# Optimization experiments

Hardware: AMD Instinct MI355X
Metric: run time of the kernel (lower is better)

Reference implementation:

```python
import jax, jax.numpy as jnp
import numpy as np

NEG_INF = -1e30


def _rope_interleaved(x, freqs):
    # x: [B,S,H,D], freqs broadcastable [1,S,1,D]; interleaved even/odd rotation
    x0 = x[..., 0::2]
    x1 = x[..., 1::2]
    f0 = freqs[..., 0::2]
    f1 = freqs[..., 1::2]
    o0 = f0 * x0 - f1 * x1
    o1 = f1 * x0 + f0 * x1
    # interleave back: out[...,0::2]=o0, out[...,1::2]=o1
    out = jnp.stack([o0, o1], axis=-1)  # [B,S,H,D/2,2]
    return out.reshape(x.shape).astype(x.dtype)


def setup_inputs() -> dict:
    key = jax.random.key(0)
    kq, kk, kv, kf = jax.random.split(key, 4)
    B, S, H, D = 2, 2048, 16, 128
    q = jax.random.normal(kq, (B, S, H, D), dtype=jnp.float32)
    k = jax.random.normal(kk, (B, S, H, D), dtype=jnp.float32)
    v = jax.random.normal(kv, (B, S, H, D), dtype=jnp.float32)
    freqs = jax.random.normal(kf, (1, S, 1, D), dtype=jnp.float32)
    return {"q": q, "k": k, "v": v, "freqs": freqs}


def reference(q, k, v, freqs):
    # RoPE (Wan-style indexed interleaved write) on q and k
    rq = _rope_interleaved(q, freqs)  # [B,S,H,D]
    rk = _rope_interleaved(k, freqs)
    B, S, H, D = q.shape
    scale = 1.0 / jnp.sqrt(jnp.asarray(D, dtype=q.dtype))
    # transpose(1,2) -> [B,H,S,D]; fused into einsum subscripts
    scores = jnp.einsum("bqhd,bkhd->bhqk", rq, rk) * scale  # [B,H,S,S]
    causal = jnp.tril(jnp.ones((S, S), dtype=bool))
    scores = jnp.where(causal[None, None, :, :], scores, NEG_INF)
    probs = jax.nn.softmax(scores, axis=-1)
    out = jnp.einsum("bhqk,bkhd->bhqd", probs, v)  # [B,H,S,D]
    return out
```

## Files before the change

### kernel.cpp

```cpp
#include <hip/hip_runtime.h>
#include <hip/hip_bf16.h>

#define B_  2
#define S_  2048
#define H_  16
#define D_  128
#define BQ  128
#define SH  (H_ * D_)
#define NT  (S_ / 64)
#define NTQ (S_ / BQ)
#define TILE_US 8192

typedef __attribute__((ext_vector_type(8))) short bf16x8;
typedef __attribute__((ext_vector_type(4))) float f32x4;
typedef __attribute__((ext_vector_type(4))) unsigned int u32x4;

__device__ __forceinline__ ushort f2bf(float x) {
  union { float f; unsigned u; } c; c.f = x;
  unsigned u = c.u;
  return (ushort)((u + 0x7FFFu + ((u >> 16) & 1u)) >> 16);
}

__device__ __forceinline__ void gload_lds16(const ushort* g, ushort* l) {
  __builtin_amdgcn_global_load_lds((const __attribute__((address_space(1))) void*)g,
                                   (__attribute__((address_space(3))) void*)l,
                                   16, 0, 0);
}

__device__ __forceinline__ bf16x8 ntload8(const ushort* p) {
  union { u32x4 u; bf16x8 v; } c;
  c.u = __builtin_nontemporal_load((const u32x4*)p);
  return c.v;
}

__device__ __forceinline__ unsigned cvt_pk_bf16(float lo, float hi) {
  unsigned d;
  asm("v_cvt_pk_bf16_f32 %0, %1, %2" : "=v"(d) : "v"(lo), "v"(hi));
  return d;
}

__global__ __launch_bounds__(256)
void pack_all(const float* __restrict__ qg, const float* __restrict__ kg,
              const float* __restrict__ vg, const float* __restrict__ fg,
              ushort* __restrict__ qr, ushort* __restrict__ kr,
              ushort* __restrict__ vt) {
  __shared__ float sv[64][133];
  const int bhp = blockIdx.x;
  const int t   = blockIdx.y;
  const int b   = bhp >> 4;
  const int h   = bhp & 15;
  const int tid = threadIdx.x;
  const float QS = 0.08838834764831845f * 1.4426950408889634f;
  const size_t tbase = ((size_t)(b * H_ + h) * NT + t) * TILE_US;

  #pragma unroll
  for (int c = 0; c < 4; c++) {
    const int idx = tid + 256 * c;
    const int row = idx >> 4;
    const int cu  = idx & 15;
    const int col = cu * 8;
    const int s   = t * 64 + row;
    const size_t goff = ((size_t)(b * S_ + s)) * SH + (size_t)h * D_ + col;

    const float4 f0 = *(const float4*)(fg + (size_t)s * D_ + col);
    const float4 f1 = *(const float4*)(fg + (size_t)s * D_ + col + 4);
    const float4 qx0 = *(const float4*)(qg + goff);
    const float4 qx1 = *(const float4*)(qg + goff + 4);
    const float4 kx0 = *(const float4*)(kg + goff);
    const float4 kx1 = *(const float4*)(kg + goff + 4);
    const float4 vx0 = *(const float4*)(vg + goff);
    const float4 vx1 = *(const float4*)(vg + goff + 4);

    *(float4*)&sv[row][col]     = vx0;
    *(float4*)&sv[row][col + 4] = vx1;

    union { ushort s[8]; uint4 v; } pq, pk;
    pq.s[0] = f2bf((f0.x*qx0.x - f0.y*qx0.y) * QS);
    pq.s[1] = f2bf((f0.y*qx0.x + f0.x*qx0.y) * QS);
    pq.s[2] = f2bf((f0.z*qx0.z - f0.w*qx0.w) * QS);
    pq.s[3] = f2bf((f0.w*qx0.z + f0.z*qx0.w) * QS);
    pq.s[4] = f2bf((f1.x*qx1.x - f1.y*qx1.y) * QS);
    pq.s[5] = f2bf((f1.y*qx1.x + f1.x*qx1.y) * QS);
    pq.s[6] = f2bf((f1.z*qx1.z - f1.w*qx1.w) * QS);
    pq.s[7] = f2bf((f1.w*qx1.z + f1.z*qx1.w) * QS);
    pk.s[0] = f2bf(f0.x*kx0.x - f0.y*kx0.y);
    pk.s[1] = f2bf(f0.y*kx0.x + f0.x*kx0.y);
    pk.s[2] = f2bf(f0.z*kx0.z - f0.w*kx0.w);
    pk.s[3] = f2bf(f0.w*kx0.z + f0.z*kx0.w);
    pk.s[4] = f2bf(f1.x*kx1.x - f1.y*kx1.y);
    pk.s[5] = f2bf(f1.y*kx1.x + f1.x*kx1.y);
    pk.s[6] = f2bf(f1.z*kx1.z - f1.w*kx1.w);
    pk.s[7] = f2bf(f1.w*kx1.z + f1.z*kx1.w);

    const int pos = ((cu >> 2) * 4 + (row >> 4)) * 64 + ((row & 15) | ((cu & 3) << 4));
    *(uint4*)(qr + tbase + (size_t)pos * 8) = pq.v;
    *(uint4*)(kr + tbase + (size_t)pos * 8) = pk.v;
  }
  __syncthreads();

  #pragma unroll
  for (int c = 0; c < 4; c++) {
    const int u2  = tid + 256 * c;
    const int g2  = u2 >> 6;
    const int ln  = u2 & 63;
    const int dim = (g2 & 7) * 16 + (ln & 15);
    const int ks2 = g2 >> 3;
    const int qd  = ln >> 4;
    union { ushort s[8]; uint4 v; } p;
    #pragma unroll
    for (int j = 0; j < 8; j++) {
      const int key = ks2 * 32 + (j >> 2) * 16 + qd * 4 + (j & 3);
      p.s[j] = f2bf(sv[key][dim]);
    }
    *(uint4*)(vt + tbase + (size_t)u2 * 8) = p.v;
  }
}

__global__ __launch_bounds__(256, 2)
void fattn4(const ushort* __restrict__ qr, const ushort* __restrict__ kr,
            const ushort* __restrict__ vt, float* __restrict__ og) {
  __shared__ __align__(16) ushort sK[2][TILE_US];

  const int bh_  = blockIdx.x;
  const int qt   = NTQ - 1 - (int)blockIdx.y;
  const int tid  = threadIdx.x;
  const int wv   = tid >> 6;
  const int lane = tid & 63;
  const int l15  = lane & 15;
  const int quad = lane >> 4;

  const size_t bh = (size_t)bh_;
  const ushort* ktb = kr + bh * NT * TILE_US;
  const ushort* vtb = vt + bh * NT * TILE_US;

  bf16x8 afq[2][4];
  {
    const ushort* qtb64 = qr + (bh * NT + 2 * qt + (wv >> 1)) * TILE_US;
    const int rbb = (wv & 1) * 2;
    #pragma unroll
    for (int rh = 0; rh < 2; rh++)
      #pragma unroll
      for (int ks = 0; ks < 4; ks++)
        afq[rh][ks] = ntload8(qtb64 + (size_t)((ks * 4 + rbb + rh) * 64 + lane) * 8);
  }

  float rs[2] = {0.0f, 0.0f};
  f32x4 o_acc[2][8];
  #pragma unroll
  for (int rh = 0; rh < 2; rh++)
    #pragma unroll
    for (int dt = 0; dt < 8; dt++) o_acc[rh][dt] = (f32x4)0.0f;

  #pragma unroll
  for (int c = 0; c < 4; c++) {
    const int g = wv * 4 + c;
    gload_lds16(ktb + g * 512 + lane * 8, &sK[0][g * 512 + lane * 8]);
  }

  const int rowmax = qt * BQ + wv * 32 + 31;
  const int nkt = 2 * qt + 2;
  int buf = 0;
  for (int kt = 0; kt < nkt; kt++) {
    __syncthreads();

    const ushort* vsrc = vtb + (size_t)kt * TILE_US;
    bf16x8 bvv[2][8];
    #pragma unroll
    for (int ks = 0; ks < 2; ks++)
      #pragma unroll
      for (int dt = 0; dt < 8; dt++)
        bvv[ks][dt] = *(const bf16x8*)(vsrc + (size_t)((ks * 8 + dt) * 64 + lane) * 8);
    __builtin_amdgcn_sched_barrier(0);

    if (kt + 1 < nkt) {
      const ushort* ksrc = ktb + (size_t)(kt + 1) * TILE_US;
      #pragma unroll
      for (int c = 0; c < 4; c++) {
        const int g = wv * 4 + c;
        gload_lds16(ksrc + g * 512 + lane * 8, &sK[buf ^ 1][g * 512 + lane * 8]);
      }
    }

    if (kt * 64 <= rowmax) {
      f32x4 sc[2][4];
      #pragma unroll
      for (int rh = 0; rh < 2; rh++)
        #pragma unroll
        for (int nt = 0; nt < 4; nt++) sc[rh][nt] = (f32x4)0.0f;
      #pragma unroll
      for (int nt = 0; nt < 4; nt++) {
        #pragma unroll
        for (int ks = 0; ks < 4; ks++) {
          const bf16x8 bk_ = *(const bf16x8*)&sK[buf][(size_t)((ks * 4 + nt) * 64 + lane) * 8];
          sc[0][nt] = __builtin_amdgcn_mfma_f32_16x16x32_bf16(bk_, afq[0][ks], sc[0][nt], 0, 0, 0);
          sc[1][nt] = __builtin_amdgcn_mfma_f32_16x16x32_bf16(bk_, afq[1][ks], sc[1][nt], 0, 0, 0);
        }
      }

      if (kt >= 2 * qt) {
        #pragma unroll
        for (int rh = 0; rh < 2; rh++) {
          const int qg = qt * 128 + wv * 32 + rh * 16 + l15;
          #pragma unroll
          for (int nt = 0; nt < 4; nt++) {
            const int kg = kt * 64 + nt * 16 + quad * 4;
            #pragma unroll
            for (int r = 0; r < 4; r++)
              if (kg + r > qg) sc[rh][nt][r] = -1e30f;
          }
        }
      }

      bf16x8 ap[2][2];
      #pragma unroll
      for (int rh = 0; rh < 2; rh++) {
        float p[4][4];
        #pragma unroll
        for (int nt = 0; nt < 4; nt++)
          #pragma unroll
          for (int r = 0; r < 4; r++) {
            p[nt][r] = __builtin_amdgcn_exp2f(sc[rh][nt][r]);
            rs[rh] += p[nt][r];
          }
        #pragma unroll
        for (int ks = 0; ks < 2; ks++) {
          union { unsigned u[4]; bf16x8 v; } pk_;
          #pragma unroll
          for (int m = 0; m < 4; m++) {
            const int nt = ks * 2 + (m >> 1);
            pk_.u[m] = cvt_pk_bf16(p[nt][2 * (m & 1)], p[nt][2 * (m & 1) + 1]);
          }
          ap[rh][ks] = pk_.v;
        }
      }

      #pragma unroll
      for (int dt = 0; dt < 8; dt++) {
        #pragma unroll
        for (int ks = 0; ks < 2; ks++) {
          o_acc[0][dt] = __builtin_amdgcn_mfma_f32_16x16x32_bf16(ap[0][ks], bvv[ks][dt], o_acc[0][dt], 0, 0, 0);
          o_acc[1][dt] = __builtin_amdgcn_mfma_f32_16x16x32_bf16(ap[1][ks], bvv[ks][dt], o_acc[1][dt], 0, 0, 0);
        }
      }
    }

    buf ^= 1;
  }

  float* ob = og + (bh * S_ + (size_t)qt * BQ) * D_;
  #pragma unroll
  for (int rh = 0; rh < 2; rh++) {
    float t = rs[rh];
    t += __shfl_xor(t, 16);
    t += __shfl_xor(t, 32);
    #pragma unroll
    for (int r = 0; r < 4; r++) {
      const float inv = 1.0f / __shfl(t, quad * 4 + r);
      const int row = wv * 32 + rh * 16 + quad * 4 + r;
      #pragma unroll
      for (int dt = 0; dt < 8; dt++)
        __builtin_nontemporal_store(o_acc[rh][dt][r] * inv,
                                    &ob[(size_t)row * D_ + dt * 16 + l15]);
    }
  }
}

extern "C" void kernel_launch(void* const* d_in, const int* in_sizes, int n_in,
                              void* d_out, int out_size, void* d_ws, size_t ws_size,
                              hipStream_t stream) {
  const float* q = (const float*)d_in[0];
  const float* k = (const float*)d_in[1];
  const float* v = (const float*)d_in[2];
  const float* f = (const float*)d_in[3];
  float* o = (float*)d_out;

  const size_t NELT = (size_t)B_ * S_ * H_ * D_;
  ushort* qr = (ushort*)d_ws;
  ushort* kr = qr + NELT;
  ushort* vt = kr + NELT;

  pack_all<<<dim3(B_ * H_, NT), dim3(256), 0, stream>>>(q, k, v, f, qr, kr, vt);
  fattn4<<<dim3(B_ * H_, NTQ), dim3(256), 0, stream>>>(qr, kr, vt, o);
}
```

Measured before the change: 191.9 us.

## Prefetch V tiles into registers one iteration ahead with manual waitcnt barrier

The attention loop now loads the next V tile into a second register buffer while the current tile is computed, alternating two buffers through a loop manually unrolled by two. The plain `__syncthreads` is replaced by an explicit `s_waitcnt vmcnt(16)` plus `s_barrier`, so the K tile load into LDS must finish while the newer V loads may still be in flight. The aim is to hide global-memory latency for V behind the QK and PV MFMA work. In exchange it doubles the V register footprint, which risks spills or lower occupancy, and it relies on hand-counted outstanding-load numbers being correct.

After: 256.2 us. 1.33x slower.

```diff
diff --git a/kernel.cpp b/kernel.cpp
--- a/kernel.cpp
+++ b/kernel.cpp
@@ -116,6 +116,96 @@
   }
 }
 
+__device__ __forceinline__ void fa_body(
+    int kt, int nkt, int qt, int wv, int lane, int l15, int quad, int rowmax,
+    const ushort* __restrict__ ktb, const ushort* __restrict__ vtb,
+    ushort (*sK)[TILE_US],
+    bf16x8 (&cur)[2][8], bf16x8 (&nxt)[2][8], bf16x8 (&afq)[2][4],
+    float (&rs)[2], f32x4 (&o_acc)[2][8]) {
+  asm volatile("s_waitcnt vmcnt(16)" ::: "memory");
+  __builtin_amdgcn_s_barrier();
+  __builtin_amdgcn_sched_barrier(0);
+
+  if (kt + 1 < nkt) {
+    const ushort* ksrc = ktb + (size_t)(kt + 1) * TILE_US;
+    #pragma unroll
+    for (int c = 0; c < 4; c++) {
+      const int g = wv * 4 + c;
+      gload_lds16(ksrc + g * 512 + lane * 8, &sK[(kt + 1) & 1][g * 512 + lane * 8]);
+    }
+    const ushort* vsrc = vtb + (size_t)(kt + 1) * TILE_US;
+    #pragma unroll
+    for (int ks = 0; ks < 2; ks++)
+      #pragma unroll
+      for (int dt = 0; dt < 8; dt++)
+        nxt[ks][dt] = *(const bf16x8*)(vsrc + (size_t)((ks * 8 + dt) * 64 + lane) * 8);
+  }
+  __builtin_amdgcn_sched_barrier(0);
+
+  if (kt * 64 <= rowmax) {
+    f32x4 sc[2][4];
+    #pragma unroll
+    for (int rh = 0; rh < 2; rh++)
+      #pragma unroll
+      for (int nt = 0; nt < 4; nt++) sc[rh][nt] = (f32x4)0.0f;
+    #pragma unroll
+    for (int nt = 0; nt < 4; nt++) {
+      #pragma unroll
+      for (int ks = 0; ks < 4; ks++) {
+        const bf16x8 bk_ = *(const bf16x8*)&sK[kt & 1][(size_t)((ks * 4 + nt) * 64 + lane) * 8];
+        sc[0][nt] = __builtin_amdgcn_mfma_f32_16x16x32_bf16(bk_, afq[0][ks], sc[0][nt], 0, 0, 0);
+        sc[1][nt] = __builtin_amdgcn_mfma_f32_16x16x32_bf16(bk_, afq[1][ks], sc[1][nt], 0, 0, 0);
+      }
+    }
+
+    if (kt >= 2 * qt) {
+      #pragma unroll
+      for (int rh = 0; rh < 2; rh++) {
+        const int qg = qt * 128 + wv * 32 + rh * 16 + l15;
+        #pragma unroll
+        for (int nt = 0; nt < 4; nt++) {
+          const int kg = kt * 64 + nt * 16 + quad * 4;
+          #pragma unroll
+          for (int r = 0; r < 4; r++)
+            if (kg + r > qg) sc[rh][nt][r] = -1e30f;
+        }
+      }
+    }
+
+    bf16x8 ap[2][2];
+    #pragma unroll
+    for (int rh = 0; rh < 2; rh++) {
+      float p[4][4];
+      #pragma unroll
+      for (int nt = 0; nt < 4; nt++)
+        #pragma unroll
+        for (int r = 0; r < 4; r++) {
+          p[nt][r] = __builtin_amdgcn_exp2f(sc[rh][nt][r]);
+          rs[rh] += p[nt][r];
+        }
+      #pragma unroll
+      for (int ks = 0; ks < 2; ks++) {
+        union { unsigned u[4]; bf16x8 v; } pk_;
+        #pragma unroll
+        for (int m = 0; m < 4; m++) {
+          const int nt = ks * 2 + (m >> 1);
+          pk_.u[m] = cvt_pk_bf16(p[nt][2 * (m & 1)], p[nt][2 * (m & 1) + 1]);
+        }
+        ap[rh][ks] = pk_.v;
+      }
+    }
+
+    #pragma unroll
+    for (int dt = 0; dt < 8; dt++) {
+      #pragma unroll
+      for (int ks = 0; ks < 2; ks++) {
+        o_acc[0][dt] = __builtin_amdgcn_mfma_f32_16x16x32_bf16(ap[0][ks], cur[ks][dt], o_acc[0][dt], 0, 0, 0);
+        o_acc[1][dt] = __builtin_amdgcn_mfma_f32_16x16x32_bf16(ap[1][ks], cur[ks][dt], o_acc[1][dt], 0, 0, 0);
+      }
+    }
+  }
+}
+
 __global__ __launch_bounds__(256, 2)
 void fattn4(const ushort* __restrict__ qr, const ushort* __restrict__ kr,
             const ushort* __restrict__ vt, float* __restrict__ og) {
@@ -156,95 +246,18 @@
     const int g = wv * 4 + c;
     gload_lds16(ktb + g * 512 + lane * 8, &sK[0][g * 512 + lane * 8]);
   }
+  bf16x8 bvvA[2][8], bvvB[2][8];
+  #pragma unroll
+  for (int ks = 0; ks < 2; ks++)
+    #pragma unroll
+    for (int dt = 0; dt < 8; dt++)
+      bvvA[ks][dt] = *(const bf16x8*)(vtb + (size_t)((ks * 8 + dt) * 64 + lane) * 8);
 
   const int rowmax = qt * BQ + wv * 32 + 31;
   const int nkt = 2 * qt + 2;
-  int buf = 0;
-  for (int kt = 0; kt < nkt; kt++) {
-    __syncthreads();
-
-    const ushort* vsrc = vtb + (size_t)kt * TILE_US;
-    bf16x8 bvv[2][8];
-    #pragma unroll
-    for (int ks = 0; ks < 2; ks++)
-      #pragma unroll
-      for (int dt = 0; dt < 8; dt++)
-        bvv[ks][dt] = *(const bf16x8*)(vsrc + (size_t)((ks * 8 + dt) * 64 + lane) * 8);
-    __builtin_amdgcn_sched_barrier(0);
-
-    if (kt + 1 < nkt) {
-      const ushort* ksrc = ktb + (size_t)(kt + 1) * TILE_US;
-      #pragma unroll
-      for (int c = 0; c < 4; c++) {
-        const int g = wv * 4 + c;
-        gload_lds16(ksrc + g * 512 + lane * 8, &sK[buf ^ 1][g * 512 + lane * 8]);
-      }
-    }
-
-    if (kt * 64 <= rowmax) {
-      f32x4 sc[2][4];
-      #pragma unroll
-      for (int rh = 0; rh < 2; rh++)
-        #pragma unroll
-        for (int nt = 0; nt < 4; nt++) sc[rh][nt] = (f32x4)0.0f;
-      #pragma unroll
-      for (int nt = 0; nt < 4; nt++) {
-        #pragma unroll
-        for (int ks = 0; ks < 4; ks++) {
-          const bf16x8 bk_ = *(const bf16x8*)&sK[buf][(size_t)((ks * 4 + nt) * 64 + lane) * 8];
-          sc[0][nt] = __builtin_amdgcn_mfma_f32_16x16x32_bf16(bk_, afq[0][ks], sc[0][nt], 0, 0, 0);
-          sc[1][nt] = __builtin_amdgcn_mfma_f32_16x16x32_bf16(bk_, afq[1][ks], sc[1][nt], 0, 0, 0);
-        }
-      }
-
-      if (kt >= 2 * qt) {
-        #pragma unroll
-        for (int rh = 0; rh < 2; rh++) {
-          const int qg = qt * 128 + wv * 32 + rh * 16 + l15;
-          #pragma unroll
-          for (int nt = 0; nt < 4; nt++) {
-            const int kg = kt * 64 + nt * 16 + quad * 4;
-            #pragma unroll
-            for (int r = 0; r < 4; r++)
-              if (kg + r > qg) sc[rh][nt][r] = -1e30f;
-          }
-        }
-      }
-
-      bf16x8 ap[2][2];
-      #pragma unroll
-      for (int rh = 0; rh < 2; rh++) {
-        float p[4][4];
-        #pragma unroll
-        for (int nt = 0; nt < 4; nt++)
-          #pragma unroll
-          for (int r = 0; r < 4; r++) {
-            p[nt][r] = __builtin_amdgcn_exp2f(sc[rh][nt][r]);
-            rs[rh] += p[nt][r];
-          }
-        #pragma unroll
-        for (int ks = 0; ks < 2; ks++) {
-          union { unsigned u[4]; bf16x8 v; } pk_;
-          #pragma unroll
-          for (int m = 0; m < 4; m++) {
-            const int nt = ks * 2 + (m >> 1);
-            pk_.u[m] = cvt_pk_bf16(p[nt][2 * (m & 1)], p[nt][2 * (m & 1) + 1]);
-          }
-          ap[rh][ks] = pk_.v;
-        }
-      }
-
-      #pragma unroll
-      for (int dt = 0; dt < 8; dt++) {
-        #pragma unroll
-        for (int ks = 0; ks < 2; ks++) {
-          o_acc[0][dt] = __builtin_amdgcn_mfma_f32_16x16x32_bf16(ap[0][ks], bvv[ks][dt], o_acc[0][dt], 0, 0, 0);
-          o_acc[1][dt] = __builtin_amdgcn_mfma_f32_16x16x32_bf16(ap[1][ks], bvv[ks][dt], o_acc[1][dt], 0, 0, 0);
-        }
-      }
-    }
-
-    buf ^= 1;
+  for (int kt = 0; kt < nkt; kt += 2) {
+    fa_body(kt,     nkt, qt, wv, lane, l15, quad, rowmax, ktb, vtb, sK, bvvA, bvvB, afq, rs, o_acc);
+    fa_body(kt + 1, nkt, qt, wv, lane, l15, quad, rowmax, ktb, vtb, sK, bvvB, bvvA, afq, rs, o_acc);
   }
 
   float* ob = og + (bh * S_ + (size_t)qt * BQ) * D_;
```

## Double query tile to 256 rows per block with 64 rows per wave

Applied to the files above, without the earlier changes.

Each block now handles 256 query rows and each wave owns 64 rows (four 16-row groups), so every K tile staged in LDS and every V fragment loaded is reused across twice as many rows. This halves the grid to 256 blocks and sets launch bounds to one block per SM. The costs are more accumulator registers per wave (o_acc 4x8 f32x4), fewer concurrent blocks, and coarser causal load balance. Waves skip the V load and compute for tiles past their own diagonal.

Result: slower. 226.0 us (+17.7%).

```diff
diff --git a/kernel.cpp b/kernel.cpp
--- a/kernel.cpp
+++ b/kernel.cpp
@@ -5,10 +5,9 @@
 #define S_  2048
 #define H_  16
 #define D_  128
-#define BQ  128
 #define SH  (H_ * D_)
 #define NT  (S_ / 64)
-#define NTQ (S_ / BQ)
+#define NQ3 (S_ / 256)
 #define TILE_US 8192
 
 typedef __attribute__((ext_vector_type(8))) short bf16x8;
@@ -116,13 +115,13 @@
   }
 }
 
-__global__ __launch_bounds__(256, 2)
-void fattn4(const ushort* __restrict__ qr, const ushort* __restrict__ kr,
+__global__ __launch_bounds__(256, 1)
+void fattn1(const ushort* __restrict__ qr, const ushort* __restrict__ kr,
             const ushort* __restrict__ vt, float* __restrict__ og) {
   __shared__ __align__(16) ushort sK[2][TILE_US];
 
   const int bh_  = blockIdx.x;
-  const int qt   = NTQ - 1 - (int)blockIdx.y;
+  const int qt   = NQ3 - 1 - (int)blockIdx.y;
   const int tid  = threadIdx.x;
   const int wv   = tid >> 6;
   const int lane = tid & 63;
@@ -133,21 +132,20 @@
   const ushort* ktb = kr + bh * NT * TILE_US;
   const ushort* vtb = vt + bh * NT * TILE_US;
 
-  bf16x8 afq[2][4];
+  bf16x8 afq[4][4];
   {
-    const ushort* qtb64 = qr + (bh * NT + 2 * qt + (wv >> 1)) * TILE_US;
-    const int rbb = (wv & 1) * 2;
-    #pragma unroll
-    for (int rh = 0; rh < 2; rh++)
+    const ushort* qtb = qr + (bh * NT + 4 * qt + wv) * TILE_US;
+    #pragma unroll
+    for (int rh = 0; rh < 4; rh++)
       #pragma unroll
       for (int ks = 0; ks < 4; ks++)
-        afq[rh][ks] = ntload8(qtb64 + (size_t)((ks * 4 + rbb + rh) * 64 + lane) * 8);
-  }
-
-  float rs[2] = {0.0f, 0.0f};
-  f32x4 o_acc[2][8];
-  #pragma unroll
-  for (int rh = 0; rh < 2; rh++)
+        afq[rh][ks] = ntload8(qtb + (size_t)((ks * 4 + rh) * 64 + lane) * 8);
+  }
+
+  float rs[4] = {0.0f, 0.0f, 0.0f, 0.0f};
+  f32x4 o_acc[4][8];
+  #pragma unroll
+  for (int rh = 0; rh < 4; rh++)
     #pragma unroll
     for (int dt = 0; dt < 8; dt++) o_acc[rh][dt] = (f32x4)0.0f;
 
@@ -157,19 +155,22 @@
     gload_lds16(ktb + g * 512 + lane * 8, &sK[0][g * 512 + lane * 8]);
   }
 
-  const int rowmax = qt * BQ + wv * 32 + 31;
-  const int nkt = 2 * qt + 2;
+  const int dtile = 4 * qt + wv;
+  const int nkt = 4 * qt + 4;
   int buf = 0;
   for (int kt = 0; kt < nkt; kt++) {
     __syncthreads();
 
-    const ushort* vsrc = vtb + (size_t)kt * TILE_US;
     bf16x8 bvv[2][8];
-    #pragma unroll
-    for (int ks = 0; ks < 2; ks++)
-      #pragma unroll
-      for (int dt = 0; dt < 8; dt++)
-        bvv[ks][dt] = *(const bf16x8*)(vsrc + (size_t)((ks * 8 + dt) * 64 + lane) * 8);
+    const bool live = (kt <= dtile);
+    if (live) {
+      const ushort* vsrc = vtb + (size_t)kt * TILE_US;
+      #pragma unroll
+      for (int ks = 0; ks < 2; ks++)
+        #pragma unroll
+        for (int dt = 0; dt < 8; dt++)
+          bvv[ks][dt] = *(const bf16x8*)(vsrc + (size_t)((ks * 8 + dt) * 64 + lane) * 8);
+    }
     __builtin_amdgcn_sched_barrier(0);
 
     if (kt + 1 < nkt) {
@@ -181,10 +182,10 @@
       }
     }
 
-    if (kt * 64 <= rowmax) {
-      f32x4 sc[2][4];
-      #pragma unroll
-      for (int rh = 0; rh < 2; rh++)
+    if (live) {
+      f32x4 sc[4][4];
+      #pragma unroll
+      for (int rh = 0; rh < 4; rh++)
         #pragma unroll
         for (int nt = 0; nt < 4; nt++) sc[rh][nt] = (f32x4)0.0f;
       #pragma unroll
@@ -192,15 +193,16 @@
         #pragma unroll
         for (int ks = 0; ks < 4; ks++) {
           const bf16x8 bk_ = *(const bf16x8*)&sK[buf][(size_t)((ks * 4 + nt) * 64 + lane) * 8];
-          sc[0][nt] = __builtin_amdgcn_mfma_f32_16x16x32_bf16(bk_, afq[0][ks], sc[0][nt], 0, 0, 0);
-          sc[1][nt] = __builtin_amdgcn_mfma_f32_16x16x32_bf16(bk_, afq[1][ks], sc[1][nt], 0, 0, 0);
-        }
-      }
-
-      if (kt >= 2 * qt) {
-        #pragma unroll
-        for (int rh = 0; rh < 2; rh++) {
-          const int qg = qt * 128 + wv * 32 + rh * 16 + l15;
+          #pragma unroll
+          for (int rh = 0; rh < 4; rh++)
+            sc[rh][nt] = __builtin_amdgcn_mfma_f32_16x16x32_bf16(bk_, afq[rh][ks], sc[rh][nt], 0, 0, 0);
+        }
+      }
+
+      if (kt == dtile) {
+        #pragma unroll
+        for (int rh = 0; rh < 4; rh++) {
+          const int qg = qt * 256 + wv * 64 + rh * 16 + l15;
           #pragma unroll
           for (int nt = 0; nt < 4; nt++) {
             const int kg = kt * 64 + nt * 16 + quad * 4;
@@ -211,9 +213,9 @@
         }
       }
 
-      bf16x8 ap[2][2];
-      #pragma unroll
-      for (int rh = 0; rh < 2; rh++) {
+      bf16x8 ap[4][2];
+      #pragma unroll
+      for (int rh = 0; rh < 4; rh++) {
         float p[4][4];
         #pragma unroll
         for (int nt = 0; nt < 4; nt++)
@@ -238,8 +240,9 @@
       for (int dt = 0; dt < 8; dt++) {
         #pragma unroll
         for (int ks = 0; ks < 2; ks++) {
-          o_acc[0][dt] = __builtin_amdgcn_mfma_f32_16x16x32_bf16(ap[0][ks], bvv[ks][dt], o_acc[0][dt], 0, 0, 0);
-          o_acc[1][dt] = __builtin_amdgcn_mfma_f32_16x16x32_bf16(ap[1][ks], bvv[ks][dt], o_acc[1][dt], 0, 0, 0);
+          #pragma unroll
+          for (int rh = 0; rh < 4; rh++)
+            o_acc[rh][dt] = __builtin_amdgcn_mfma_f32_16x16x32_bf16(ap[rh][ks], bvv[ks][dt], o_acc[rh][dt], 0, 0, 0);
         }
       }
     }
@@ -247,16 +250,16 @@
     buf ^= 1;
   }
 
-  float* ob = og + (bh * S_ + (size_t)qt * BQ) * D_;
-  #pragma unroll
-  for (int rh = 0; rh < 2; rh++) {
+  float* ob = og + (bh * S_ + (size_t)qt * 256) * D_;
+  #pragma unroll
+  for (int rh = 0; rh < 4; rh++) {
     float t = rs[rh];
     t += __shfl_xor(t, 16);
     t += __shfl_xor(t, 32);
     #pragma unroll
     for (int r = 0; r < 4; r++) {
       const float inv = 1.0f / __shfl(t, quad * 4 + r);
-      const int row = wv * 32 + rh * 16 + quad * 4 + r;
+      const int row = wv * 64 + rh * 16 + quad * 4 + r;
       #pragma unroll
       for (int dt = 0; dt < 8; dt++)
         __builtin_nontemporal_store(o_acc[rh][dt][r] * inv,
@@ -280,5 +283,5 @@
   ushort* vt = kr + NELT;
 
   pack_all<<<dim3(B_ * H_, NT), dim3(256), 0, stream>>>(q, k, v, f, qr, kr, vt);
-  fattn4<<<dim3(B_ * H_, NTQ), dim3(256), 0, stream>>>(qr, kr, vt, o);
-}
+  fattn1<<<dim3(B_ * H_, NQ3), dim3(256), 0, stream>>>(qr, kr, vt, o);
+}
```
